# Kernel optimization log

Hardware: AMD Instinct MI355X
Metric: run time of the kernel (lower is better)

Reference implementation:

```python
import jax, jax.numpy as jnp
import numpy as np

DIM = 1024
NUM_HEADS = 16
SCALE = DIM ** (-0.5)  # NOTE: source scales by full dim, not head_dim


def setup_inputs() -> dict:
    key = jax.random.key(0)
    ks = jax.random.split(key, 10)
    B, N, C = 2, 2048, DIM
    s = 0.02
    return {
        "x": jax.random.normal(ks[0], (B, N, C), dtype=jnp.float32),
        "queries": jax.random.normal(ks[1], (B, N, C), dtype=jnp.float32),
        "wq": jax.random.normal(ks[2], (C, C), dtype=jnp.float32) * s,
        "bq": jnp.zeros((C,), dtype=jnp.float32),
        "wk": jax.random.normal(ks[3], (C, C), dtype=jnp.float32) * s,
        "bk": jnp.zeros((C,), dtype=jnp.float32),
        "wv": jax.random.normal(ks[4], (C, C), dtype=jnp.float32) * s,
        "bv": jnp.zeros((C,), dtype=jnp.float32),
        "wo": jax.random.normal(ks[5], (C, C), dtype=jnp.float32) * s,
        "bo": jnp.zeros((C,), dtype=jnp.float32),
    }


def reference(x, queries, wq, bq, wk, bk, wv, bv, wo, bo):
    B, N, C = queries.shape
    H = NUM_HEADS
    D = C // H
    # torch Linear: y = x @ W.T + b  (W is [out, in])
    q = (queries @ wq.T + bq).reshape(B, N, H, D).transpose(0, 2, 1, 3)  # [B,H,N,D]
    k = (x @ wk.T + bk).reshape(B, N, H, D).transpose(0, 2, 1, 3)
    v = (x @ wv.T + bv).reshape(B, N, H, D).transpose(0, 2, 1, 3)
    attn = jnp.einsum("bhqd,bhkd->bhqk", q, k) * SCALE  # full-dim scale per source
    attn = jax.nn.softmax(attn, axis=-1)
    out = jnp.einsum("bhqk,bhkd->bhqd", attn, v)  # [B,H,N,D]
    out = out.transpose(0, 2, 1, 3).reshape(B, N, C)
    return out @ wo.T + bo
```

## Files before the change

kernel.cpp:

```cpp
#include <hip/hip_runtime.h>
#include <hip/hip_bf16.h>

typedef __attribute__((ext_vector_type(8))) short bf16x8;
typedef __attribute__((ext_vector_type(4))) float f32x4;
typedef unsigned short u16;
typedef unsigned int u32;

#define MFMA16(a,b,c) __builtin_amdgcn_mfma_f32_16x16x32_bf16((a),(b),(c),0,0,0)

#if defined(__has_builtin) && __has_builtin(__builtin_amdgcn_exp2f)
#define EXP2(x) __builtin_amdgcn_exp2f(x)
#else
#define EXP2(x) exp2f(x)
#endif

#define QSCALE 0.045084220027780106f

__device__ __forceinline__ u16 f2bf(float f) {
  union { float f; unsigned int u; } v; v.f = f;
  unsigned int r = v.u + 0x7FFFu + ((v.u >> 16) & 1u);
  return (u16)(r >> 16);
}

__device__ __forceinline__ u32 pkbf(float a, float b) {
  union { __hip_bfloat162 h; u32 u; } cv;
  cv.h = __float22bfloat162_rn(make_float2(a, b));
  return cv.u;
}

__device__ __forceinline__ void gld16(const void* g, void* l) {
  __builtin_amdgcn_global_load_lds(
      (__attribute__((address_space(1))) void*)(g),
      (__attribute__((address_space(3))) void*)(l), 16, 0, 0);
}

__global__ __launch_bounds__(256) void cast_all(
    const float* __restrict__ x, const float* __restrict__ qu,
    const float* __restrict__ wq, const float* __restrict__ wk,
    const float* __restrict__ wv, const float* __restrict__ wo,
    u16* __restrict__ xb, u16* __restrict__ qub,
    u16* __restrict__ wqb, u16* __restrict__ wkb,
    u16* __restrict__ wvb, u16* __restrict__ wob)
{
  int i = blockIdx.x * 256 + threadIdx.x;
  const float4* src; u16* dst; int off;
  if (i < 1048576)      { src = (const float4*)qu; dst = qub; off = i; }
  else if (i < 2097152) { src = (const float4*)x;  dst = xb;  off = i - 1048576; }
  else if (i < 2359296) { src = (const float4*)wq; dst = wqb; off = i - 2097152; }
  else if (i < 2621440) { src = (const float4*)wk; dst = wkb; off = i - 2359296; }
  else if (i < 2883584) { src = (const float4*)wv; dst = wvb; off = i - 2621440; }
  else                  { src = (const float4*)wo; dst = wob; off = i - 2883584; }
  float4 v = src[off];
  ushort4 r; r.x = f2bf(v.x); r.y = f2bf(v.y); r.z = f2bf(v.z); r.w = f2bf(v.w);
  ((ushort4*)dst)[off] = r;
}

__global__ __launch_bounds__(256) void gemm_qkv(
    const u16* __restrict__ qub, const u16* __restrict__ xb,
    const u16* __restrict__ wqb, const u16* __restrict__ wkb, const u16* __restrict__ wvb,
    const float* __restrict__ bq, const float* __restrict__ bk, const float* __restrict__ bv,
    u16* __restrict__ qhd, u16* __restrict__ khd, u16* __restrict__ vtd)
{
  __shared__ u16 As[128 * 64];
  __shared__ u16 Bs[128 * 64];
  int tid = threadIdx.x, w = tid >> 6, lane = tid & 63;
  int c = lane & 15, quad = lane >> 4;
  int bm = blockIdx.x, bn = blockIdx.y, z = blockIdx.z;
  int wm = w >> 1, wn = w & 1;
  const u16* A = (z == 0) ? qub : xb;
  const u16* W = (z == 0) ? wqb : (z == 1) ? wkb : wvb;
  f32x4 acc[4][4] = {};
  for (int k0 = 0; k0 < 1024; k0 += 64) {
#pragma unroll
    for (int i = 0; i < 4; i++) {
      int seg = i * 256 + w * 64 + lane;
      int row = seg >> 3, pseg = seg & 7;
      int lseg = pseg ^ (row & 7);
      gld16(A + (size_t)(bm * 128 + row) * 1024 + k0 + lseg * 8,
            &As[(i * 256 + w * 64) * 8]);
      gld16(W + (size_t)(bn * 128 + row) * 1024 + k0 + lseg * 8,
            &Bs[(i * 256 + w * 64) * 8]);
    }
    __syncthreads();
#pragma unroll
    for (int ks = 0; ks < 2; ks++) {
      bf16x8 af[4], bfr[4];
#pragma unroll
      for (int mt = 0; mt < 4; mt++) {
        int row = wm * 64 + mt * 16 + c;
        int cseg = (ks * 4 + quad) ^ (row & 7);
        af[mt] = *(const bf16x8*)&As[(row * 8 + cseg) * 8];
      }
#pragma unroll
      for (int nt = 0; nt < 4; nt++) {
        int row = wn * 64 + nt * 16 + c;
        int cseg = (ks * 4 + quad) ^ (row & 7);
        bfr[nt] = *(const bf16x8*)&Bs[(row * 8 + cseg) * 8];
      }
      if (z < 2) {
#pragma unroll
        for (int ct = 0; ct < 4; ct++)
#pragma unroll
          for (int tt = 0; tt < 4; tt++)
            acc[ct][tt] = MFMA16(bfr[ct], af[tt], acc[ct][tt]);
      } else {
#pragma unroll
        for (int mt = 0; mt < 4; mt++)
#pragma unroll
          for (int nt = 0; nt < 4; nt++)
            acc[mt][nt] = MFMA16(af[mt], bfr[nt], acc[mt][nt]);
      }
    }
    __syncthreads();
  }
  if (z < 2) {
    const float* bias = (z == 0) ? bq : bk;
    u16* dst = (z == 0) ? qhd : khd;
    float sc = (z == 0) ? QSCALE : 1.0f;
    float4 bbs[4];
#pragma unroll
    for (int ct = 0; ct < 4; ct++) {
      float4 b4 = *(const float4*)&bias[bn * 128 + wn * 64 + ct * 16 + quad * 4];
      bbs[ct].x = b4.x * sc; bbs[ct].y = b4.y * sc;
      bbs[ct].z = b4.z * sc; bbs[ct].w = b4.w * sc;
    }
#pragma unroll
    for (int ct = 0; ct < 4; ct++) {
      int ch = bn * 128 + wn * 64 + ct * 16 + quad * 4;
      int h = ch >> 6, d0 = ch & 63;
#pragma unroll
      for (int tt = 0; tt < 4; tt++) {
        int tok = bm * 128 + wm * 64 + tt * 16 + c;
        int b = tok >> 11, n = tok & 2047;
        float v0 = fmaf(acc[ct][tt][0], sc, bbs[ct].x);
        float v1 = fmaf(acc[ct][tt][1], sc, bbs[ct].y);
        float v2 = fmaf(acc[ct][tt][2], sc, bbs[ct].z);
        float v3 = fmaf(acc[ct][tt][3], sc, bbs[ct].w);
        uint2 pk; pk.x = pkbf(v0, v1); pk.y = pkbf(v2, v3);
        *(uint2*)&dst[((size_t)(b * 16 + h) * 2048 + n) * 64 + d0] = pk;
      }
    }
  } else {
    float bval[4];
#pragma unroll
    for (int nt = 0; nt < 4; nt++)
      bval[nt] = bv[bn * 128 + wn * 64 + nt * 16 + c];
#pragma unroll
    for (int mt = 0; mt < 4; mt++) {
      int tokl = (mt & 2) * 16 + quad * 8 + (mt & 1) * 4;
      int tok = bm * 128 + wm * 64 + tokl;
      int b = tok >> 11, np = tok & 2047;
#pragma unroll
      for (int nt = 0; nt < 4; nt++) {
        int ch = bn * 128 + wn * 64 + nt * 16 + c;
        int h = ch >> 6, d = ch & 63;
        float v0 = acc[mt][nt][0] + bval[nt];
        float v1 = acc[mt][nt][1] + bval[nt];
        float v2 = acc[mt][nt][2] + bval[nt];
        float v3 = acc[mt][nt][3] + bval[nt];
        uint2 pk; pk.x = pkbf(v0, v1); pk.y = pkbf(v2, v3);
        *(uint2*)&vtd[((size_t)(b * 16 + h) * 64 + d) * 2048 + np] = pk;
      }
    }
  }
}

__global__ __launch_bounds__(128) void attn(
    const u16* __restrict__ qh, const u16* __restrict__ kh,
    const u16* __restrict__ vt, u16* __restrict__ ot)
{
  __shared__ u16 Kbuf[2][64 * 64];
  __shared__ u16 Vbuf[2][64 * 64];
  int tid = threadIdx.x, w = tid >> 6, lane = tid & 63;
  int c = lane & 15, quad = lane >> 4;
  int bh = blockIdx.x, qt = blockIdx.y;
  const u16* qp = qh + ((size_t)bh * 2048 + qt * 64 + w * 32) * 64;

  bf16x8 Qf[2][2];
#pragma unroll
  for (int qt2 = 0; qt2 < 2; qt2++)
#pragma unroll
    for (int ks = 0; ks < 2; ks++)
      Qf[qt2][ks] = *(const bf16x8*)(qp + (size_t)(qt2 * 16 + c) * 64 + ks * 32 + quad * 8);

  int off0 = c * 64 + ((quad) ^ (c & 7)) * 8;
  int off1 = c * 64 + ((4 + quad) ^ (c & 7)) * 8;

  int sr = lane >> 3;
  int row0 = w * 8 + sr;
  int sls = (lane & 7) ^ (sr & 7);
  const u16* kg = kh + (size_t)bh * 2048 * 64 + row0 * 64 + sls * 8;
  const u16* vg = vt + (size_t)bh * 64 * 2048 + row0 * 2048 + sls * 8;

#define STAGE(B)                                                                \
  {                                                                             \
    gld16(kg,          &Kbuf[B][(w * 64) * 8]);                                 \
    gld16(kg + 1024,   &Kbuf[B][(128 + w * 64) * 8]);                           \
    gld16(kg + 2048,   &Kbuf[B][(256 + w * 64) * 8]);                           \
    gld16(kg + 3072,   &Kbuf[B][(384 + w * 64) * 8]);                           \
    gld16(vg,          &Vbuf[B][(w * 64) * 8]);                                 \
    gld16(vg + 32768,  &Vbuf[B][(128 + w * 64) * 8]);                           \
    gld16(vg + 65536,  &Vbuf[B][(256 + w * 64) * 8]);                           \
    gld16(vg + 98304,  &Vbuf[B][(384 + w * 64) * 8]);                           \
    kg += 4096; vg += 64;                                                       \
  }

  STAGE(0)
  __syncthreads();

  f32x4 O[2][4] = {};
  f32x4 Lacc[2] = {};
  bf16x8 vone;
#pragma unroll
  for (int j = 0; j < 8; j++) vone[j] = (short)0x3F80;

#define ITER(PH, PREF)                                                          \
  {                                                                             \
    if (PREF) STAGE(PH ^ 1)                                                     \
    const u16* Ks = Kbuf[PH];                                                   \
    const u16* Vs = Vbuf[PH];                                                   \
    bf16x8 Kf[4][2];                                                            \
    _Pragma("unroll") for (int nt = 0; nt < 4; nt++) {                          \
      Kf[nt][0] = *(const bf16x8*)&Ks[off0 + nt * 1024];                        \
      Kf[nt][1] = *(const bf16x8*)&Ks[off1 + nt * 1024];                        \
    }                                                                           \
    f32x4 S[2][4] = {};                                                         \
    _Pragma("unroll") for (int qt2 = 0; qt2 < 2; qt2++)                         \
      _Pragma("unroll") for (int nt = 0; nt < 4; nt++) {                        \
        S[qt2][nt] = MFMA16(Kf[nt][0], Qf[qt2][0], S[qt2][nt]);                 \
        S[qt2][nt] = MFMA16(Kf[nt][1], Qf[qt2][1], S[qt2][nt]);                 \
      }                                                                         \
    bf16x8 pa[2][2];                                                            \
    _Pragma("unroll") for (int qt2 = 0; qt2 < 2; qt2++)                         \
      _Pragma("unroll") for (int i = 0; i < 2; i++) {                           \
        float e0 = EXP2(S[qt2][2 * i][0]), e1 = EXP2(S[qt2][2 * i][1]);         \
        float e2 = EXP2(S[qt2][2 * i][2]), e3 = EXP2(S[qt2][2 * i][3]);         \
        float e4 = EXP2(S[qt2][2 * i + 1][0]), e5 = EXP2(S[qt2][2 * i + 1][1]); \
        float e6 = EXP2(S[qt2][2 * i + 1][2]), e7 = EXP2(S[qt2][2 * i + 1][3]); \
        union { uint4 u; bf16x8 v; } cv;                                        \
        cv.u.x = pkbf(e0, e1); cv.u.y = pkbf(e2, e3);                           \
        cv.u.z = pkbf(e4, e5); cv.u.w = pkbf(e6, e7);                           \
        pa[qt2][i] = cv.v;                                                      \
      }                                                                         \
    Lacc[0] = MFMA16(pa[0][0], vone, Lacc[0]);                                  \
    Lacc[0] = MFMA16(pa[0][1], vone, Lacc[0]);                                  \
    Lacc[1] = MFMA16(pa[1][0], vone, Lacc[1]);                                  \
    Lacc[1] = MFMA16(pa[1][1], vone, Lacc[1]);                                  \
    bf16x8 Vf[4][2];                                                            \
    _Pragma("unroll") for (int dt = 0; dt < 4; dt++) {                          \
      Vf[dt][0] = *(const bf16x8*)&Vs[off0 + dt * 1024];                        \
      Vf[dt][1] = *(const bf16x8*)&Vs[off1 + dt * 1024];                        \
    }                                                                           \
    _Pragma("unroll") for (int qt2 = 0; qt2 < 2; qt2++)                         \
      _Pragma("unroll") for (int dt = 0; dt < 4; dt++) {                        \
        O[qt2][dt] = MFMA16(pa[qt2][0], Vf[dt][0], O[qt2][dt]);                 \
        O[qt2][dt] = MFMA16(pa[qt2][1], Vf[dt][1], O[qt2][dt]);                 \
      }                                                                         \
    __syncthreads();                                                            \
  }

  for (int kt2 = 0; kt2 < 15; kt2++) {
    ITER(0, 1)
    ITER(1, 1)
  }
  ITER(0, 1)
  ITER(1, 0)
#undef ITER
#undef STAGE

  int b_ = bh >> 4, h = bh & 15;
#pragma unroll
  for (int qt2 = 0; qt2 < 2; qt2++) {
    f32x4 linv;
#pragma unroll
    for (int j = 0; j < 4; j++) linv[j] = 1.0f / Lacc[qt2][j];
#pragma unroll
    for (int j = 0; j < 4; j++) {
      int n = qt * 64 + w * 32 + qt2 * 16 + quad * 4 + j;
      u16* op = ot + (((size_t)b_ * 2048 + n) * 16 + h) * 64;
#pragma unroll
      for (int dt = 0; dt < 4; dt++)
        op[dt * 16 + c] = f2bf(O[qt2][dt][j] * linv[j]);
    }
  }
}

__global__ __launch_bounds__(256) void gemm_out(
    const u16* __restrict__ Aot, const u16* __restrict__ wob,
    const float* __restrict__ bo, float* __restrict__ out)
{
  __shared__ u16 As[64 * 64];
  __shared__ u16 Bs[128 * 64];
  int tid = threadIdx.x, w = tid >> 6, lane = tid & 63;
  int bm = blockIdx.x, bn = blockIdx.y;
  int wm = w >> 1, wn = w & 1;
  f32x4 acc[2][4] = {};
  for (int k0 = 0; k0 < 1024; k0 += 64) {
#pragma unroll
    for (int i = 0; i < 2; i++) {
      int seg = i * 256 + tid;
      int row = seg >> 3, pseg = seg & 7;
      int lseg = pseg ^ (row & 7);
      gld16(Aot + (size_t)(bm * 64 + row) * 1024 + k0 + lseg * 8,
            &As[(i * 256 + tid - (tid & 7)) * 8 + (tid & 7) * 8]);
    }
#pragma unroll
    for (int i = 0; i < 4; i++) {
      int seg = i * 256 + tid;
      int row = seg >> 3, pseg = seg & 7;
      int lseg = pseg ^ (row & 7);
      gld16(wob + (size_t)(bn * 128 + row) * 1024 + k0 + lseg * 8,
            &Bs[(i * 256 + tid - (tid & 7)) * 8 + (tid & 7) * 8]);
    }
    __syncthreads();
#pragma unroll
    for (int ks = 0; ks < 2; ks++) {
      bf16x8 af[2], bfr[4];
#pragma unroll
      for (int mt = 0; mt < 2; mt++) {
        int row = wm * 32 + mt * 16 + (lane & 15);
        int cseg = (ks * 4 + (lane >> 4)) ^ (row & 7);
        af[mt] = *(const bf16x8*)&As[(row * 8 + cseg) * 8];
      }
#pragma unroll
      for (int nt = 0; nt < 4; nt++) {
        int row = wn * 64 + nt * 16 + (lane & 15);
        int cseg = (ks * 4 + (lane >> 4)) ^ (row & 7);
        bfr[nt] = *(const bf16x8*)&Bs[(row * 8 + cseg) * 8];
      }
#pragma unroll
      for (int mt = 0; mt < 2; mt++)
#pragma unroll
        for (int nt = 0; nt < 4; nt++)
          acc[mt][nt] = MFMA16(af[mt], bfr[nt], acc[mt][nt]);
    }
    __syncthreads();
  }
#pragma unroll
  for (int nt = 0; nt < 4; nt++) {
    int o = bn * 128 + wn * 64 + nt * 16 + (lane & 15);
    float bval = bo[o];
#pragma unroll
    for (int mt = 0; mt < 2; mt++)
#pragma unroll
      for (int j = 0; j < 4; j++) {
        int m = bm * 64 + wm * 32 + mt * 16 + (lane >> 4) * 4 + j;
        out[(size_t)m * 1024 + o] = acc[mt][nt][j] + bval;
      }
  }
}

extern "C" void kernel_launch(void* const* d_in, const int* in_sizes, int n_in,
                              void* d_out, int out_size, void* d_ws, size_t ws_size,
                              hipStream_t stream)
{
  const float* x  = (const float*)d_in[0];
  const float* qu = (const float*)d_in[1];
  const float* wq = (const float*)d_in[2];
  const float* bq = (const float*)d_in[3];
  const float* wk = (const float*)d_in[4];
  const float* bk = (const float*)d_in[5];
  const float* wv = (const float*)d_in[6];
  const float* bv = (const float*)d_in[7];
  const float* wo = (const float*)d_in[8];
  const float* bo = (const float*)d_in[9];
  float* out = (float*)d_out;
  char* ws = (char*)d_ws;
  u16* xb  = (u16*)(ws + (size_t)0);
  u16* qub = (u16*)(ws + ((size_t)8  << 20));
  u16* wqb = (u16*)(ws + ((size_t)16 << 20));
  u16* wkb = (u16*)(ws + ((size_t)18 << 20));
  u16* wvb = (u16*)(ws + ((size_t)20 << 20));
  u16* wob = (u16*)(ws + ((size_t)22 << 20));
  u16* qhd = (u16*)(ws + ((size_t)24 << 20));
  u16* khd = (u16*)(ws + ((size_t)32 << 20));
  u16* vtd = (u16*)(ws + ((size_t)40 << 20));
  u16* otd = (u16*)(ws + ((size_t)48 << 20));

  cast_all<<<12288, 256, 0, stream>>>(x, qu, wq, wk, wv, wo,
                                      xb, qub, wqb, wkb, wvb, wob);
  gemm_qkv<<<dim3(32, 8, 3), 256, 0, stream>>>(qub, xb, wqb, wkb, wvb,
                                               bq, bk, bv, qhd, khd, vtd);
  attn<<<dim3(32, 32), 128, 0, stream>>>(qhd, khd, vtd, otd);
  gemm_out<<<dim3(64, 8), 256, 0, stream>>>(otd, wob, bo, out);
}
```

Measured before the change: 204.6 us.

## Restructure attention into single-wave blocks with software-pipelined QK and PV stages

Attention now runs as one 64-thread wave per block handling 32 queries, with 32-key tiles double-buffered in LDS, using waitcnt-based synchronisation instead of __syncthreads. The loop is software-pipelined so the QK^T MFMAs for the next tile are issued alongside the exp and PV MFMAs for the current tile. This targets barrier stalls and the serial QK→softmax→PV dependency. In exchange, K/V are reloaded by twice as many blocks, and correctness depends on hand-written vmcnt accounting with no barrier, since a single wave owns all its LDS.

```diff
diff --git a/kernel.cpp b/kernel.cpp
--- a/kernel.cpp
+++ b/kernel.cpp
@@ -165,17 +165,17 @@
   }
 }
 
-__global__ __launch_bounds__(128) void attn(
+__global__ __launch_bounds__(64, 2) void attn(
     const u16* __restrict__ qh, const u16* __restrict__ kh,
     const u16* __restrict__ vt, u16* __restrict__ ot)
 {
-  __shared__ u16 Kbuf[2][64 * 64];
-  __shared__ u16 Vbuf[2][64 * 64];
-  int tid = threadIdx.x, w = tid >> 6, lane = tid & 63;
+  __shared__ u16 Kbuf[2][32 * 64];
+  __shared__ u16 Vbuf[2][64 * 32];
+  int lane = threadIdx.x;
   int c = lane & 15, quad = lane >> 4;
   int bh = blockIdx.x, qt = blockIdx.y;
-  const u16* qp = qh + ((size_t)bh * 2048 + qt * 64 + w * 32) * 64;
-
+
+  const u16* qp = qh + ((size_t)bh * 2048 + qt * 32) * 64;
   bf16x8 Qf[2][2];
 #pragma unroll
   for (int qt2 = 0; qt2 < 2; qt2++)
@@ -183,89 +183,139 @@
     for (int ks = 0; ks < 2; ks++)
       Qf[qt2][ks] = *(const bf16x8*)(qp + (size_t)(qt2 * 16 + c) * 64 + ks * 32 + quad * 8);
 
-  int off0 = c * 64 + ((quad) ^ (c & 7)) * 8;
-  int off1 = c * 64 + ((4 + quad) ^ (c & 7)) * 8;
-
-  int sr = lane >> 3;
-  int row0 = w * 8 + sr;
-  int sls = (lane & 7) ^ (sr & 7);
-  const u16* kg = kh + (size_t)bh * 2048 * 64 + row0 * 64 + sls * 8;
-  const u16* vg = vt + (size_t)bh * 64 * 2048 + row0 * 2048 + sls * 8;
+  int r8 = lane >> 3;
+  int ks8 = (lane & 7) ^ r8;
+  int r4 = lane >> 2;
+  int vs4 = (lane & 3) ^ ((lane >> 3) & 3);
+  const u16* kg = kh + (size_t)bh * 131072 + r8 * 64 + ks8 * 8;
+  const u16* vg = vt + (size_t)bh * 131072 + r4 * 2048 + vs4 * 8;
+
+  int offK0 = c * 64 + ((quad)     ^ (c & 7)) * 8;
+  int offK1 = c * 64 + ((4 + quad) ^ (c & 7)) * 8;
+  int offV  = c * 32 + ((quad ^ ((c >> 1) & 3)) * 8);
 
 #define STAGE(B)                                                                \
   {                                                                             \
-    gld16(kg,          &Kbuf[B][(w * 64) * 8]);                                 \
-    gld16(kg + 1024,   &Kbuf[B][(128 + w * 64) * 8]);                           \
-    gld16(kg + 2048,   &Kbuf[B][(256 + w * 64) * 8]);                           \
-    gld16(kg + 3072,   &Kbuf[B][(384 + w * 64) * 8]);                           \
-    gld16(vg,          &Vbuf[B][(w * 64) * 8]);                                 \
-    gld16(vg + 32768,  &Vbuf[B][(128 + w * 64) * 8]);                           \
-    gld16(vg + 65536,  &Vbuf[B][(256 + w * 64) * 8]);                           \
-    gld16(vg + 98304,  &Vbuf[B][(384 + w * 64) * 8]);                           \
-    kg += 4096; vg += 64;                                                       \
-  }
-
-  STAGE(0)
-  __syncthreads();
+    asm volatile("s_waitcnt lgkmcnt(0)" ::: "memory");                          \
+    gld16(kg,         &Kbuf[B][0]);                                             \
+    gld16(kg + 512,   &Kbuf[B][512]);                                           \
+    gld16(kg + 1024,  &Kbuf[B][1024]);                                          \
+    gld16(kg + 1536,  &Kbuf[B][1536]);                                          \
+    gld16(vg,         &Vbuf[B][0]);                                             \
+    gld16(vg + 32768, &Vbuf[B][512]);                                           \
+    gld16(vg + 65536, &Vbuf[B][1024]);                                          \
+    gld16(vg + 98304, &Vbuf[B][1536]);                                          \
+    kg += 2048; vg += 32;                                                       \
+  }
 
   f32x4 O[2][4] = {};
   f32x4 Lacc[2] = {};
+  f32x4 SA[2][2], SB[2][2];
+  bf16x8 VfA[4], VfB[4];
   bf16x8 vone;
 #pragma unroll
   for (int j = 0; j < 8; j++) vone[j] = (short)0x3F80;
 
-#define ITER(PH, PREF)                                                          \
+#define BUILD0(Sx, Vfx, PH)                                                     \
   {                                                                             \
-    if (PREF) STAGE(PH ^ 1)                                                     \
     const u16* Ks = Kbuf[PH];                                                   \
     const u16* Vs = Vbuf[PH];                                                   \
-    bf16x8 Kf[4][2];                                                            \
-    _Pragma("unroll") for (int nt = 0; nt < 4; nt++) {                          \
-      Kf[nt][0] = *(const bf16x8*)&Ks[off0 + nt * 1024];                        \
-      Kf[nt][1] = *(const bf16x8*)&Ks[off1 + nt * 1024];                        \
+    bf16x8 Kf0 = *(const bf16x8*)&Ks[offK0];                                    \
+    bf16x8 Kf1 = *(const bf16x8*)&Ks[offK1];                                    \
+    bf16x8 Kf2 = *(const bf16x8*)&Ks[offK0 + 1024];                             \
+    bf16x8 Kf3 = *(const bf16x8*)&Ks[offK1 + 1024];                             \
+    Vfx[0] = *(const bf16x8*)&Vs[offV];                                         \
+    Vfx[1] = *(const bf16x8*)&Vs[offV + 512];                                   \
+    Vfx[2] = *(const bf16x8*)&Vs[offV + 1024];                                  \
+    Vfx[3] = *(const bf16x8*)&Vs[offV + 1536];                                  \
+    f32x4 zz = {};                                                              \
+    Sx[0][0] = MFMA16(Kf1, Qf[0][1], MFMA16(Kf0, Qf[0][0], zz));                \
+    Sx[0][1] = MFMA16(Kf3, Qf[0][1], MFMA16(Kf2, Qf[0][0], zz));                \
+    Sx[1][0] = MFMA16(Kf1, Qf[1][1], MFMA16(Kf0, Qf[1][0], zz));                \
+    Sx[1][1] = MFMA16(Kf3, Qf[1][1], MFMA16(Kf2, Qf[1][0], zz));                \
+  }
+
+#define HALF(Scur, Vfcur, Snxt, Vfnxt, PHNXT)                                   \
+  {                                                                             \
+    const u16* Ks = Kbuf[PHNXT];                                                \
+    const u16* Vs = Vbuf[PHNXT];                                                \
+    bf16x8 Kf0 = *(const bf16x8*)&Ks[offK0];                                    \
+    bf16x8 Kf1 = *(const bf16x8*)&Ks[offK1];                                    \
+    bf16x8 Kf2 = *(const bf16x8*)&Ks[offK0 + 1024];                             \
+    bf16x8 Kf3 = *(const bf16x8*)&Ks[offK1 + 1024];                             \
+    Vfnxt[0] = *(const bf16x8*)&Vs[offV];                                       \
+    Vfnxt[1] = *(const bf16x8*)&Vs[offV + 512];                                 \
+    Vfnxt[2] = *(const bf16x8*)&Vs[offV + 1024];                                \
+    Vfnxt[3] = *(const bf16x8*)&Vs[offV + 1536];                                \
+    bf16x8 pa[2];                                                               \
+    _Pragma("unroll") for (int q2 = 0; q2 < 2; q2++) {                          \
+      float e0 = EXP2(Scur[q2][0][0]), e1 = EXP2(Scur[q2][0][1]);               \
+      float e2 = EXP2(Scur[q2][0][2]), e3 = EXP2(Scur[q2][0][3]);               \
+      float e4 = EXP2(Scur[q2][1][0]), e5 = EXP2(Scur[q2][1][1]);               \
+      float e6 = EXP2(Scur[q2][1][2]), e7 = EXP2(Scur[q2][1][3]);               \
+      union { uint4 u; bf16x8 v; } cv;                                          \
+      cv.u.x = pkbf(e0, e1); cv.u.y = pkbf(e2, e3);                             \
+      cv.u.z = pkbf(e4, e5); cv.u.w = pkbf(e6, e7);                             \
+      pa[q2] = cv.v;                                                            \
     }                                                                           \
-    f32x4 S[2][4] = {};                                                         \
-    _Pragma("unroll") for (int qt2 = 0; qt2 < 2; qt2++)                         \
-      _Pragma("unroll") for (int nt = 0; nt < 4; nt++) {                        \
-        S[qt2][nt] = MFMA16(Kf[nt][0], Qf[qt2][0], S[qt2][nt]);                 \
-        S[qt2][nt] = MFMA16(Kf[nt][1], Qf[qt2][1], S[qt2][nt]);                 \
-      }                                                                         \
-    bf16x8 pa[2][2];                                                            \
-    _Pragma("unroll") for (int qt2 = 0; qt2 < 2; qt2++)                         \
-      _Pragma("unroll") for (int i = 0; i < 2; i++) {                           \
-        float e0 = EXP2(S[qt2][2 * i][0]), e1 = EXP2(S[qt2][2 * i][1]);         \
-        float e2 = EXP2(S[qt2][2 * i][2]), e3 = EXP2(S[qt2][2 * i][3]);         \
-        float e4 = EXP2(S[qt2][2 * i + 1][0]), e5 = EXP2(S[qt2][2 * i + 1][1]); \
-        float e6 = EXP2(S[qt2][2 * i + 1][2]), e7 = EXP2(S[qt2][2 * i + 1][3]); \
-        union { uint4 u; bf16x8 v; } cv;                                        \
-        cv.u.x = pkbf(e0, e1); cv.u.y = pkbf(e2, e3);                           \
-        cv.u.z = pkbf(e4, e5); cv.u.w = pkbf(e6, e7);                           \
-        pa[qt2][i] = cv.v;                                                      \
-      }                                                                         \
-    Lacc[0] = MFMA16(pa[0][0], vone, Lacc[0]);                                  \
-    Lacc[0] = MFMA16(pa[0][1], vone, Lacc[0]);                                  \
-    Lacc[1] = MFMA16(pa[1][0], vone, Lacc[1]);                                  \
-    Lacc[1] = MFMA16(pa[1][1], vone, Lacc[1]);                                  \
-    bf16x8 Vf[4][2];                                                            \
-    _Pragma("unroll") for (int dt = 0; dt < 4; dt++) {                          \
-      Vf[dt][0] = *(const bf16x8*)&Vs[off0 + dt * 1024];                        \
-      Vf[dt][1] = *(const bf16x8*)&Vs[off1 + dt * 1024];                        \
+    f32x4 zz = {};                                                              \
+    Snxt[0][0] = MFMA16(Kf1, Qf[0][1], MFMA16(Kf0, Qf[0][0], zz));              \
+    Snxt[0][1] = MFMA16(Kf3, Qf[0][1], MFMA16(Kf2, Qf[0][0], zz));              \
+    Snxt[1][0] = MFMA16(Kf1, Qf[1][1], MFMA16(Kf0, Qf[1][0], zz));              \
+    Snxt[1][1] = MFMA16(Kf3, Qf[1][1], MFMA16(Kf2, Qf[1][0], zz));              \
+    Lacc[0] = MFMA16(pa[0], vone, Lacc[0]);                                     \
+    Lacc[1] = MFMA16(pa[1], vone, Lacc[1]);                                     \
+    _Pragma("unroll") for (int q2 = 0; q2 < 2; q2++)                            \
+      _Pragma("unroll") for (int dt = 0; dt < 4; dt++)                          \
+        O[q2][dt] = MFMA16(pa[q2], Vfcur[dt], O[q2][dt]);                       \
+  }
+
+#define FIN(Scur, Vfcur)                                                        \
+  {                                                                             \
+    bf16x8 pa[2];                                                               \
+    _Pragma("unroll") for (int q2 = 0; q2 < 2; q2++) {                          \
+      float e0 = EXP2(Scur[q2][0][0]), e1 = EXP2(Scur[q2][0][1]);               \
+      float e2 = EXP2(Scur[q2][0][2]), e3 = EXP2(Scur[q2][0][3]);               \
+      float e4 = EXP2(Scur[q2][1][0]), e5 = EXP2(Scur[q2][1][1]);               \
+      float e6 = EXP2(Scur[q2][1][2]), e7 = EXP2(Scur[q2][1][3]);               \
+      union { uint4 u; bf16x8 v; } cv;                                          \
+      cv.u.x = pkbf(e0, e1); cv.u.y = pkbf(e2, e3);                             \
+      cv.u.z = pkbf(e4, e5); cv.u.w = pkbf(e6, e7);                             \
+      pa[q2] = cv.v;                                                            \
     }                                                                           \
-    _Pragma("unroll") for (int qt2 = 0; qt2 < 2; qt2++)                         \
-      _Pragma("unroll") for (int dt = 0; dt < 4; dt++) {                        \
-        O[qt2][dt] = MFMA16(pa[qt2][0], Vf[dt][0], O[qt2][dt]);                 \
-        O[qt2][dt] = MFMA16(pa[qt2][1], Vf[dt][1], O[qt2][dt]);                 \
-      }                                                                         \
-    __syncthreads();                                                            \
-  }
-
-  for (int kt2 = 0; kt2 < 15; kt2++) {
-    ITER(0, 1)
-    ITER(1, 1)
-  }
-  ITER(0, 1)
-  ITER(1, 0)
-#undef ITER
+    Lacc[0] = MFMA16(pa[0], vone, Lacc[0]);                                     \
+    Lacc[1] = MFMA16(pa[1], vone, Lacc[1]);                                     \
+    _Pragma("unroll") for (int q2 = 0; q2 < 2; q2++)                            \
+      _Pragma("unroll") for (int dt = 0; dt < 4; dt++)                          \
+        O[q2][dt] = MFMA16(pa[q2], Vfcur[dt], O[q2][dt]);                       \
+  }
+
+#define WAITV8                                                                  \
+  asm volatile("s_waitcnt vmcnt(8)" ::: "memory");                              \
+  __builtin_amdgcn_sched_barrier(0);
+
+  STAGE(0)
+  STAGE(1)
+  WAITV8
+  BUILD0(SA, VfA, 0)
+
+  for (int hp = 0; hp < 31; hp++) {
+    STAGE(0)
+    WAITV8
+    HALF(SA, VfA, SB, VfB, 1)
+    STAGE(1)
+    WAITV8
+    HALF(SB, VfB, SA, VfA, 0)
+  }
+  asm volatile("s_waitcnt vmcnt(0)" ::: "memory");
+  __builtin_amdgcn_sched_barrier(0);
+  HALF(SA, VfA, SB, VfB, 1)
+  FIN(SB, VfB)
+
+#undef WAITV8
+#undef FIN
+#undef HALF
+#undef BUILD0
 #undef STAGE
 
   int b_ = bh >> 4, h = bh & 15;
@@ -276,7 +326,7 @@
     for (int j = 0; j < 4; j++) linv[j] = 1.0f / Lacc[qt2][j];
 #pragma unroll
     for (int j = 0; j < 4; j++) {
-      int n = qt * 64 + w * 32 + qt2 * 16 + quad * 4 + j;
+      int n = qt * 32 + qt2 * 16 + quad * 4 + j;
       u16* op = ot + (((size_t)b_ * 2048 + n) * 16 + h) * 64;
 #pragma unroll
       for (int dt = 0; dt < 4; dt++)
@@ -381,6 +431,6 @@
                                       xb, qub, wqb, wkb, wvb, wob);
   gemm_qkv<<<dim3(32, 8, 3), 256, 0, stream>>>(qub, xb, wqb, wkb, wvb,
                                                bq, bk, bv, qhd, khd, vtd);
-  attn<<<dim3(32, 32), 128, 0, stream>>>(qhd, khd, vtd, otd);
+  attn<<<dim3(32, 64), 64, 0, stream>>>(qhd, khd, vtd, otd);
   gemm_out<<<dim3(64, 8), 256, 0, stream>>>(otd, wob, bo, out);
 }
```

Result: slower. 210.0 us (+2.6%).

## Split attention over key halves with larger query tiles and a combine kernel

Applied to the files above, without the earlier changes.

The attention kernel now uses 256-thread blocks covering 128 queries and splits the key range in two across blockIdx.z. Each block therefore shares its staged K/V tiles across four waves instead of two, and runs half as many key iterations. Each split writes unnormalised fp32 partial outputs and row sums, and a new combine kernel adds them, normalises, and packs the result to bf16 in the layout gemm_out expects. The aim is more K/V reuse and more waves in flight per block, at the cost of extra fp32 partial traffic to global memory and one more kernel launch. Workspace regions whose inputs are no longer needed are reused for the partial buffers.

```diff
diff --git a/kernel.cpp b/kernel.cpp
--- a/kernel.cpp
+++ b/kernel.cpp
@@ -165,16 +165,18 @@
   }
 }
 
-__global__ __launch_bounds__(128) void attn(
+__global__ __launch_bounds__(256, 4) void attn(
     const u16* __restrict__ qh, const u16* __restrict__ kh,
-    const u16* __restrict__ vt, u16* __restrict__ ot)
+    const u16* __restrict__ vt,
+    float* __restrict__ op0, float* __restrict__ op1,
+    float* __restrict__ lp0, float* __restrict__ lp1)
 {
   __shared__ u16 Kbuf[2][64 * 64];
   __shared__ u16 Vbuf[2][64 * 64];
   int tid = threadIdx.x, w = tid >> 6, lane = tid & 63;
   int c = lane & 15, quad = lane >> 4;
-  int bh = blockIdx.x, qt = blockIdx.y;
-  const u16* qp = qh + ((size_t)bh * 2048 + qt * 64 + w * 32) * 64;
+  int bh = blockIdx.x, qt = blockIdx.y, zs = blockIdx.z;
+  const u16* qp = qh + ((size_t)bh * 2048 + qt * 128 + w * 32) * 64;
 
   bf16x8 Qf[2][2];
 #pragma unroll
@@ -187,21 +189,17 @@
   int off1 = c * 64 + ((4 + quad) ^ (c & 7)) * 8;
 
   int sr = lane >> 3;
-  int row0 = w * 8 + sr;
+  int row0 = w * 16 + sr;
   int sls = (lane & 7) ^ (sr & 7);
-  const u16* kg = kh + (size_t)bh * 2048 * 64 + row0 * 64 + sls * 8;
-  const u16* vg = vt + (size_t)bh * 64 * 2048 + row0 * 2048 + sls * 8;
+  const u16* kg = kh + (size_t)bh * 131072 + (size_t)zs * 65536 + row0 * 64 + sls * 8;
+  const u16* vg = vt + (size_t)bh * 131072 + row0 * 2048 + zs * 1024 + sls * 8;
 
 #define STAGE(B)                                                                \
   {                                                                             \
-    gld16(kg,          &Kbuf[B][(w * 64) * 8]);                                 \
-    gld16(kg + 1024,   &Kbuf[B][(128 + w * 64) * 8]);                           \
-    gld16(kg + 2048,   &Kbuf[B][(256 + w * 64) * 8]);                           \
-    gld16(kg + 3072,   &Kbuf[B][(384 + w * 64) * 8]);                           \
-    gld16(vg,          &Vbuf[B][(w * 64) * 8]);                                 \
-    gld16(vg + 32768,  &Vbuf[B][(128 + w * 64) * 8]);                           \
-    gld16(vg + 65536,  &Vbuf[B][(256 + w * 64) * 8]);                           \
-    gld16(vg + 98304,  &Vbuf[B][(384 + w * 64) * 8]);                           \
+    gld16(kg,          &Kbuf[B][w * 1024]);                                     \
+    gld16(kg + 512,    &Kbuf[B][w * 1024 + 512]);                               \
+    gld16(vg,          &Vbuf[B][w * 1024]);                                     \
+    gld16(vg + 16384,  &Vbuf[B][w * 1024 + 512]);                               \
     kg += 4096; vg += 64;                                                       \
   }
 
@@ -259,7 +257,7 @@
     __syncthreads();                                                            \
   }
 
-  for (int kt2 = 0; kt2 < 15; kt2++) {
+  for (int kt2 = 0; kt2 < 7; kt2++) {
     ITER(0, 1)
     ITER(1, 1)
   }
@@ -268,21 +266,38 @@
 #undef ITER
 #undef STAGE
 
+  float* Op = zs ? op1 : op0;
+  float* Lp = zs ? lp1 : lp0;
+#pragma unroll
+  for (int qt2 = 0; qt2 < 2; qt2++) {
+#pragma unroll
+    for (int j = 0; j < 4; j++) {
+      int n = qt * 128 + w * 32 + qt2 * 16 + quad * 4 + j;
+      float* op = Op + ((size_t)bh * 2048 + n) * 64;
+#pragma unroll
+      for (int dt = 0; dt < 4; dt++)
+        op[dt * 16 + c] = O[qt2][dt][j];
+      if (c == 0) Lp[(size_t)bh * 2048 + n] = Lacc[qt2][j];
+    }
+  }
+}
+
+__global__ __launch_bounds__(256) void combine(
+    const float* __restrict__ op0, const float* __restrict__ op1,
+    const float* __restrict__ lp0, const float* __restrict__ lp1,
+    u16* __restrict__ ot)
+{
+  int i = blockIdx.x * 256 + threadIdx.x;
+  int d4 = i & 15, n = (i >> 4) & 2047, bh = i >> 15;
+  size_t ro = ((size_t)bh * 2048 + n);
+  float4 a = ((const float4*)op0)[ro * 16 + d4];
+  float4 b = ((const float4*)op1)[ro * 16 + d4];
+  float li = 1.0f / (lp0[ro] + lp1[ro]);
+  uint2 pk;
+  pk.x = pkbf((a.x + b.x) * li, (a.y + b.y) * li);
+  pk.y = pkbf((a.z + b.z) * li, (a.w + b.w) * li);
   int b_ = bh >> 4, h = bh & 15;
-#pragma unroll
-  for (int qt2 = 0; qt2 < 2; qt2++) {
-    f32x4 linv;
-#pragma unroll
-    for (int j = 0; j < 4; j++) linv[j] = 1.0f / Lacc[qt2][j];
-#pragma unroll
-    for (int j = 0; j < 4; j++) {
-      int n = qt * 64 + w * 32 + qt2 * 16 + quad * 4 + j;
-      u16* op = ot + (((size_t)b_ * 2048 + n) * 16 + h) * 64;
-#pragma unroll
-      for (int dt = 0; dt < 4; dt++)
-        op[dt * 16 + c] = f2bf(O[qt2][dt][j] * linv[j]);
-    }
-  }
+  *(uint2*)&ot[(((size_t)b_ * 2048 + n) * 16 + h) * 64 + d4 * 4] = pk;
 }
 
 __global__ __launch_bounds__(256) void gemm_out(
@@ -375,12 +390,17 @@
   u16* qhd = (u16*)(ws + ((size_t)24 << 20));
   u16* khd = (u16*)(ws + ((size_t)32 << 20));
   u16* vtd = (u16*)(ws + ((size_t)40 << 20));
-  u16* otd = (u16*)(ws + ((size_t)48 << 20));
+  float* op0 = (float*)(ws + (size_t)0);
+  float* op1 = (float*)(ws + ((size_t)48 << 20));
+  float* lp0 = (float*)(ws + ((size_t)16 << 20));
+  float* lp1 = (float*)(ws + ((size_t)16 << 20) + 262144);
+  u16* otd = (u16*)(ws + ((size_t)40 << 20));
 
   cast_all<<<12288, 256, 0, stream>>>(x, qu, wq, wk, wv, wo,
                                       xb, qub, wqb, wkb, wvb, wob);
   gemm_qkv<<<dim3(32, 8, 3), 256, 0, stream>>>(qub, xb, wqb, wkb, wvb,
                                                bq, bk, bv, qhd, khd, vtd);
-  attn<<<dim3(32, 32), 128, 0, stream>>>(qhd, khd, vtd, otd);
+  attn<<<dim3(32, 16, 2), 256, 0, stream>>>(qhd, khd, vtd, op0, op1, lp0, lp1);
+  combine<<<4096, 256, 0, stream>>>(op0, op1, lp0, lp1, otd);
   gemm_out<<<dim3(64, 8), 256, 0, stream>>>(otd, wob, bo, out);
 }
```

Result: slower. 217.5 us (+6.3%).

## Split attention KV range across warps with per-warp staging and LDS combine

Applied to the files above, without the earlier changes.

The attention kernel now gives each block 32 queries instead of 64, and its two warps split the 2048 keys into halves. Each warp stages its own K/V tiles through registers into private LDS buffers, which removes the block-wide barriers from the main loop. At the end, warp 1's partial O and row sums are combined with warp 0's through LDS before normalization. The grid doubles to raise occupancy, at the cost of per-warp synchronous register-to-LDS copies and reading K/V twice as often across blocks.

```diff
diff --git a/kernel.cpp b/kernel.cpp
--- a/kernel.cpp
+++ b/kernel.cpp
@@ -165,17 +165,18 @@
   }
 }
 
-__global__ __launch_bounds__(128) void attn(
+__global__ __launch_bounds__(128, 4) void attn(
     const u16* __restrict__ qh, const u16* __restrict__ kh,
     const u16* __restrict__ vt, u16* __restrict__ ot)
 {
-  __shared__ u16 Kbuf[2][64 * 64];
-  __shared__ u16 Vbuf[2][64 * 64];
+  __shared__ u16 KL[2][32 * 64];
+  __shared__ u16 VL[2][64 * 32];
+  __shared__ float CL[32];
   int tid = threadIdx.x, w = tid >> 6, lane = tid & 63;
   int c = lane & 15, quad = lane >> 4;
   int bh = blockIdx.x, qt = blockIdx.y;
-  const u16* qp = qh + ((size_t)bh * 2048 + qt * 64 + w * 32) * 64;
-
+
+  const u16* qp = qh + ((size_t)bh * 2048 + qt * 32) * 64;
   bf16x8 Qf[2][2];
 #pragma unroll
   for (int qt2 = 0; qt2 < 2; qt2++)
@@ -183,30 +184,42 @@
     for (int ks = 0; ks < 2; ks++)
       Qf[qt2][ks] = *(const bf16x8*)(qp + (size_t)(qt2 * 16 + c) * 64 + ks * 32 + quad * 8);
 
-  int off0 = c * 64 + ((quad) ^ (c & 7)) * 8;
-  int off1 = c * 64 + ((4 + quad) ^ (c & 7)) * 8;
-
-  int sr = lane >> 3;
-  int row0 = w * 8 + sr;
-  int sls = (lane & 7) ^ (sr & 7);
-  const u16* kg = kh + (size_t)bh * 2048 * 64 + row0 * 64 + sls * 8;
-  const u16* vg = vt + (size_t)bh * 64 * 2048 + row0 * 2048 + sls * 8;
-
-#define STAGE(B)                                                                \
+  int kro = (lane >> 3);
+  int ksw = ((lane & 7) ^ (kro & 7)) * 8;
+  const u16* kg = kh + (size_t)bh * 131072 + (size_t)w * 65536 + kro * 64 + ksw;
+  int kwo = (kro * 64 + (lane & 7) * 8);
+  int vro = (lane >> 2);
+  int vsw = ((lane & 3) ^ (vro & 3)) * 8;
+  const u16* vg = vt + (size_t)bh * 131072 + (size_t)vro * 2048 + w * 1024 + vsw;
+  int vwo = (vro * 32 + (lane & 3) * 8);
+
+  u16* Ks = KL[w];
+  u16* Vs = VL[w];
+
+  int offK[2][2], offV[4];
+#pragma unroll
+  for (int nt = 0; nt < 2; nt++)
+#pragma unroll
+    for (int ks = 0; ks < 2; ks++)
+      offK[nt][ks] = (nt * 16 + c) * 64 + (((ks * 4 + quad) ^ (c & 7)) & 7) * 8;
+#pragma unroll
+  for (int dt = 0; dt < 4; dt++)
+    offV[dt] = (dt * 16 + c) * 32 + ((quad ^ (c & 3)) & 3) * 8;
+
+  uint4 RK[4], RV[4];
+#define ISSUE(T)                                                                \
   {                                                                             \
-    gld16(kg,          &Kbuf[B][(w * 64) * 8]);                                 \
-    gld16(kg + 1024,   &Kbuf[B][(128 + w * 64) * 8]);                           \
-    gld16(kg + 2048,   &Kbuf[B][(256 + w * 64) * 8]);                           \
-    gld16(kg + 3072,   &Kbuf[B][(384 + w * 64) * 8]);                           \
-    gld16(vg,          &Vbuf[B][(w * 64) * 8]);                                 \
-    gld16(vg + 32768,  &Vbuf[B][(128 + w * 64) * 8]);                           \
-    gld16(vg + 65536,  &Vbuf[B][(256 + w * 64) * 8]);                           \
-    gld16(vg + 98304,  &Vbuf[B][(384 + w * 64) * 8]);                           \
-    kg += 4096; vg += 64;                                                       \
-  }
-
-  STAGE(0)
-  __syncthreads();
+    const u16* kp = kg + (T) * 2048;                                            \
+    const u16* vp = vg + (T) * 32;                                              \
+    RK[0] = *(const uint4*)(kp);                                                \
+    RK[1] = *(const uint4*)(kp + 512);                                          \
+    RK[2] = *(const uint4*)(kp + 1024);                                         \
+    RK[3] = *(const uint4*)(kp + 1536);                                         \
+    RV[0] = *(const uint4*)(vp);                                                \
+    RV[1] = *(const uint4*)(vp + 32768);                                        \
+    RV[2] = *(const uint4*)(vp + 65536);                                        \
+    RV[3] = *(const uint4*)(vp + 98304);                                        \
+  }
 
   f32x4 O[2][4] = {};
   f32x4 Lacc[2] = {};
@@ -214,73 +227,89 @@
 #pragma unroll
   for (int j = 0; j < 8; j++) vone[j] = (short)0x3F80;
 
-#define ITER(PH, PREF)                                                          \
-  {                                                                             \
-    if (PREF) STAGE(PH ^ 1)                                                     \
-    const u16* Ks = Kbuf[PH];                                                   \
-    const u16* Vs = Vbuf[PH];                                                   \
-    bf16x8 Kf[4][2];                                                            \
-    _Pragma("unroll") for (int nt = 0; nt < 4; nt++) {                          \
-      Kf[nt][0] = *(const bf16x8*)&Ks[off0 + nt * 1024];                        \
-      Kf[nt][1] = *(const bf16x8*)&Ks[off1 + nt * 1024];                        \
-    }                                                                           \
-    f32x4 S[2][4] = {};                                                         \
-    _Pragma("unroll") for (int qt2 = 0; qt2 < 2; qt2++)                         \
-      _Pragma("unroll") for (int nt = 0; nt < 4; nt++) {                        \
-        S[qt2][nt] = MFMA16(Kf[nt][0], Qf[qt2][0], S[qt2][nt]);                 \
-        S[qt2][nt] = MFMA16(Kf[nt][1], Qf[qt2][1], S[qt2][nt]);                 \
-      }                                                                         \
-    bf16x8 pa[2][2];                                                            \
-    _Pragma("unroll") for (int qt2 = 0; qt2 < 2; qt2++)                         \
-      _Pragma("unroll") for (int i = 0; i < 2; i++) {                           \
-        float e0 = EXP2(S[qt2][2 * i][0]), e1 = EXP2(S[qt2][2 * i][1]);         \
-        float e2 = EXP2(S[qt2][2 * i][2]), e3 = EXP2(S[qt2][2 * i][3]);         \
-        float e4 = EXP2(S[qt2][2 * i + 1][0]), e5 = EXP2(S[qt2][2 * i + 1][1]); \
-        float e6 = EXP2(S[qt2][2 * i + 1][2]), e7 = EXP2(S[qt2][2 * i + 1][3]); \
-        union { uint4 u; bf16x8 v; } cv;                                        \
-        cv.u.x = pkbf(e0, e1); cv.u.y = pkbf(e2, e3);                           \
-        cv.u.z = pkbf(e4, e5); cv.u.w = pkbf(e6, e7);                           \
-        pa[qt2][i] = cv.v;                                                      \
-      }                                                                         \
-    Lacc[0] = MFMA16(pa[0][0], vone, Lacc[0]);                                  \
-    Lacc[0] = MFMA16(pa[0][1], vone, Lacc[0]);                                  \
-    Lacc[1] = MFMA16(pa[1][0], vone, Lacc[1]);                                  \
-    Lacc[1] = MFMA16(pa[1][1], vone, Lacc[1]);                                  \
-    bf16x8 Vf[4][2];                                                            \
-    _Pragma("unroll") for (int dt = 0; dt < 4; dt++) {                          \
-      Vf[dt][0] = *(const bf16x8*)&Vs[off0 + dt * 1024];                        \
-      Vf[dt][1] = *(const bf16x8*)&Vs[off1 + dt * 1024];                        \
-    }                                                                           \
-    _Pragma("unroll") for (int qt2 = 0; qt2 < 2; qt2++)                         \
-      _Pragma("unroll") for (int dt = 0; dt < 4; dt++) {                        \
-        O[qt2][dt] = MFMA16(pa[qt2][0], Vf[dt][0], O[qt2][dt]);                 \
-        O[qt2][dt] = MFMA16(pa[qt2][1], Vf[dt][1], O[qt2][dt]);                 \
-      }                                                                         \
-    __syncthreads();                                                            \
-  }
-
-  for (int kt2 = 0; kt2 < 15; kt2++) {
-    ITER(0, 1)
-    ITER(1, 1)
-  }
-  ITER(0, 1)
-  ITER(1, 0)
-#undef ITER
-#undef STAGE
-
-  int b_ = bh >> 4, h = bh & 15;
-#pragma unroll
-  for (int qt2 = 0; qt2 < 2; qt2++) {
-    f32x4 linv;
-#pragma unroll
-    for (int j = 0; j < 4; j++) linv[j] = 1.0f / Lacc[qt2][j];
-#pragma unroll
-    for (int j = 0; j < 4; j++) {
-      int n = qt * 64 + w * 32 + qt2 * 16 + quad * 4 + j;
-      u16* op = ot + (((size_t)b_ * 2048 + n) * 16 + h) * 64;
+  ISSUE(0)
+
+  for (int t = 0; t < 32; t++) {
+#pragma unroll
+    for (int i = 0; i < 4; i++) {
+      *(uint4*)&Ks[i * 512 + kwo] = RK[i];
+      *(uint4*)&Vs[i * 512 + vwo] = RV[i];
+    }
+    if (t < 31) ISSUE(t + 1)
+    __builtin_amdgcn_sched_barrier(0);
+
+    bf16x8 Kf[2][2];
+#pragma unroll
+    for (int nt = 0; nt < 2; nt++) {
+      Kf[nt][0] = *(const bf16x8*)&Ks[offK[nt][0]];
+      Kf[nt][1] = *(const bf16x8*)&Ks[offK[nt][1]];
+    }
+    f32x4 S[2][2] = {};
+#pragma unroll
+    for (int qt2 = 0; qt2 < 2; qt2++)
+#pragma unroll
+      for (int nt = 0; nt < 2; nt++) {
+        S[qt2][nt] = MFMA16(Kf[nt][0], Qf[qt2][0], S[qt2][nt]);
+        S[qt2][nt] = MFMA16(Kf[nt][1], Qf[qt2][1], S[qt2][nt]);
+      }
+    bf16x8 pa[2];
+#pragma unroll
+    for (int qt2 = 0; qt2 < 2; qt2++) {
+      float e0 = EXP2(S[qt2][0][0]), e1 = EXP2(S[qt2][0][1]);
+      float e2 = EXP2(S[qt2][0][2]), e3 = EXP2(S[qt2][0][3]);
+      float e4 = EXP2(S[qt2][1][0]), e5 = EXP2(S[qt2][1][1]);
+      float e6 = EXP2(S[qt2][1][2]), e7 = EXP2(S[qt2][1][3]);
+      union { uint4 u; bf16x8 v; } cv;
+      cv.u.x = pkbf(e0, e1); cv.u.y = pkbf(e2, e3);
+      cv.u.z = pkbf(e4, e5); cv.u.w = pkbf(e6, e7);
+      pa[qt2] = cv.v;
+    }
+    Lacc[0] = MFMA16(pa[0], vone, Lacc[0]);
+    Lacc[1] = MFMA16(pa[1], vone, Lacc[1]);
+    bf16x8 Vf[4];
+#pragma unroll
+    for (int dt = 0; dt < 4; dt++)
+      Vf[dt] = *(const bf16x8*)&Vs[offV[dt]];
+#pragma unroll
+    for (int qt2 = 0; qt2 < 2; qt2++)
 #pragma unroll
       for (int dt = 0; dt < 4; dt++)
-        op[dt * 16 + c] = f2bf(O[qt2][dt][j] * linv[j]);
+        O[qt2][dt] = MFMA16(pa[qt2], Vf[dt], O[qt2][dt]);
+  }
+#undef ISSUE
+
+  __syncthreads();
+  float* CmbO = (float*)&VL[0][0];
+  if (w == 1) {
+#pragma unroll
+    for (int qt2 = 0; qt2 < 2; qt2++) {
+      if (c == 0)
+        *(f32x4*)&CL[qt2 * 16 + quad * 4] = Lacc[qt2];
+#pragma unroll
+      for (int dt = 0; dt < 4; dt++)
+#pragma unroll
+        for (int j = 0; j < 4; j++)
+          CmbO[(qt2 * 16 + quad * 4 + j) * 64 + dt * 16 + c] = O[qt2][dt][j];
+    }
+  }
+  __syncthreads();
+  if (w == 0) {
+    int b_ = bh >> 4, h = bh & 15;
+#pragma unroll
+    for (int qt2 = 0; qt2 < 2; qt2++) {
+#pragma unroll
+      for (int j = 0; j < 4; j++) {
+        int qrow = qt2 * 16 + quad * 4 + j;
+        float ltot = Lacc[qt2][j] + CL[qrow];
+        float linv = 1.0f / ltot;
+        int n = qt * 32 + qrow;
+        u16* op = ot + (((size_t)b_ * 2048 + n) * 16 + h) * 64;
+#pragma unroll
+        for (int dt = 0; dt < 4; dt++) {
+          float o = O[qt2][dt][j] + CmbO[qrow * 64 + dt * 16 + c];
+          op[dt * 16 + c] = f2bf(o * linv);
+        }
+      }
     }
   }
 }
@@ -381,6 +410,6 @@
                                       xb, qub, wqb, wkb, wvb, wob);
   gemm_qkv<<<dim3(32, 8, 3), 256, 0, stream>>>(qub, xb, wqb, wkb, wvb,
                                                bq, bk, bv, qhd, khd, vtd);
-  attn<<<dim3(32, 32), 128, 0, stream>>>(qhd, khd, vtd, otd);
+  attn<<<dim3(32, 64), 128, 0, stream>>>(qhd, khd, vtd, otd);
   gemm_out<<<dim3(64, 8), 256, 0, stream>>>(otd, wob, bo, out);
 }
```

Result: slower. 437.0 us (+113.6%).
